# Optimization experiments

Hardware: AMD Instinct MI355X
Metric: run time of the kernel (lower is better)

## Reference

```python
import jax, jax.numpy as jnp
import numpy as np

B, S, D = 4, 2048, 1024
H = 16
DH = D // H  # head dim for qk and v

def setup_inputs() -> dict:
    key = jax.random.key(0)
    ks = jax.random.split(key, 5)
    x_q = jax.random.normal(ks[0], (B, S, D), dtype=jnp.float32)
    # weights stored as [d_in, d_out] (equivalent to torch Linear weight.T)
    scale = 1.0 / np.sqrt(D)
    Wq = jax.random.normal(ks[1], (D, D), dtype=jnp.float32) * scale
    Wk = jax.random.normal(ks[2], (D, D), dtype=jnp.float32) * scale
    Wv = jax.random.normal(ks[3], (D, D), dtype=jnp.float32) * scale
    Wo = jax.random.normal(ks[4], (D, D), dtype=jnp.float32) * scale
    return {"x_q": x_q, "Wq": Wq, "Wk": Wk, "Wv": Wv, "Wo": Wo}

def reference(x_q, Wq, Wk, Wv, Wo):
    b, sq, _ = x_q.shape
    sk = sq  # self-attention: x_k = x_v = x_q
    # projections -> [b, h, s, dh]
    q = (x_q @ Wq).reshape(b, sq, H, DH).transpose(0, 2, 1, 3)
    k = (x_q @ Wk).reshape(b, sk, H, DH).transpose(0, 2, 1, 3)
    v = (x_q @ Wv).reshape(b, sk, H, DH).transpose(0, 2, 1, 3)
    # scores [b, h, sq, sk]
    scores = jnp.einsum('bhqd,bhkd->bhqk', q, k)
    # causal mask: triu(ones(sq, sk), diagonal=1 + sk - sq)
    i = jnp.arange(sq)[:, None]
    j = jnp.arange(sk)[None, :]
    mask = (j - i) >= (1 + sk - sq)
    scores = jnp.where(mask, -jnp.inf, scores)
    attn = jax.nn.softmax(scores / jnp.sqrt(jnp.float32(DH)), axis=-1)
    # dropout p=0.0 -> identity
    ctx = jnp.einsum('bhqk,bhkd->bhqd', attn, v)  # [b,h,sq,dh]
    ctx = ctx.transpose(0, 2, 1, 3).reshape(b, sq, H * DH)
    return ctx @ Wo
```

## Files before the change

kernel.cpp:

```cpp
#include <hip/hip_runtime.h>

#define S_LEN 2048
#define D_MODEL 1024
#define NH 16
#define DHEAD 64
#define BATCH 4

typedef _Float16 half8 __attribute__((ext_vector_type(8)));
typedef __fp16 fp16x2 __attribute__((ext_vector_type(2)));
typedef float floatx4 __attribute__((ext_vector_type(4)));

#define EXP2SCALE 0.1803368801111244f

__device__ __forceinline__ unsigned short f2h(float f) {
    _Float16 h = (_Float16)f;
    return __builtin_bit_cast(unsigned short, h);
}

__device__ __forceinline__ float fexp2(float x) {
    float r;
    asm("v_exp_f32 %0, %1" : "=v"(r) : "v"(x));
    return r;
}
__device__ __forceinline__ float frcp(float x) {
    float r;
    asm("v_rcp_f32 %0, %1" : "=v"(r) : "v"(x));
    return r;
}

__device__ __forceinline__ unsigned int pk2(float a, float b) {
    fp16x2 p = __builtin_amdgcn_cvt_pkrtz(a, b);
    return __builtin_bit_cast(unsigned int, p);
}

__device__ __forceinline__ void gload_lds16(const unsigned short* g, unsigned short* l) {
    __builtin_amdgcn_global_load_lds(
        (const __attribute__((address_space(1))) void*)g,
        (__attribute__((address_space(3))) void*)l,
        16, 0, 0);
}

__global__ __launch_bounds__(256) void convert_f2h_kernel(const float* __restrict__ in,
                                                          unsigned short* __restrict__ out,
                                                          int n4) {
    int i = blockIdx.x * 256 + threadIdx.x;
    if (i < n4) {
        float4 v = ((const float4*)in)[i];
        ushort4 o;
        o.x = f2h(v.x); o.y = f2h(v.y); o.z = f2h(v.z); o.w = f2h(v.w);
        ((ushort4*)out)[i] = o;
    }
}

__global__ __launch_bounds__(256) void transpose_w_kernel(const float* __restrict__ W0,
                                                          const float* __restrict__ W1,
                                                          const float* __restrict__ W2,
                                                          const float* __restrict__ W3,
                                                          unsigned short* __restrict__ T0,
                                                          unsigned short* __restrict__ T1,
                                                          unsigned short* __restrict__ T2,
                                                          unsigned short* __restrict__ T3) {
    const float* W = blockIdx.z == 0 ? W0 : blockIdx.z == 1 ? W1 : blockIdx.z == 2 ? W2 : W3;
    unsigned short* Wt = blockIdx.z == 0 ? T0 : blockIdx.z == 1 ? T1 : blockIdx.z == 2 ? T2 : T3;
    __shared__ float tile[32][33];
    int x = threadIdx.x;
    int y = threadIdx.y;
    int k0 = blockIdx.y * 32;
    int n0 = blockIdx.x * 32;
    for (int i = 0; i < 4; i++)
        tile[y + 8 * i][x] = W[(size_t)(k0 + y + 8 * i) * D_MODEL + n0 + x];
    __syncthreads();
    for (int i = 0; i < 4; i++)
        Wt[(size_t)(n0 + y + 8 * i) * D_MODEL + k0 + x] = f2h(tile[x][y + 8 * i]);
}

template<int MODE>
__device__ __forceinline__ void gemm_body(const unsigned short* __restrict__ A,
                                          const unsigned short* __restrict__ Bt,
                                          void* __restrict__ Cout,
                                          int N, int K,
                                          int bx, int by,
                                          unsigned short* smem, float osc) {
    const int tid  = threadIdx.x;
    const int wave = tid >> 6;
    const int lane = tid & 63;
    const int quad = lane >> 4;
    const int l16  = lane & 15;
    const int wm = (wave >> 1) * 64;
    const int wn = (wave & 1) * 64;
    const int tm = by * 128;
    const int tn = bx * 128;

    const int r0 = tid >> 3;
    const int g0 = (tid & 7) ^ (r0 & 7);
    const unsigned short* pA = A  + (size_t)(tm + r0) * K + g0 * 8;
    const unsigned short* pB = Bt + (size_t)(tn + r0) * K + g0 * 8;
    const int wofs = wave * 512;

    const int sK0 = (((0 << 2) | quad) ^ (l16 & 7)) << 3;
    const int sK1 = (((1 << 2) | quad) ^ (l16 & 7)) << 3;
    const int arow = wm + l16;
    const int brow = wn + l16;

    floatx4 acc[4][4] = {};
    half8 af[2][2], bf[4][2];

    {
        unsigned short* Ab = smem;
        unsigned short* Bb = smem + 8192;
        gload_lds16(pB,         Bb +        wofs);
        gload_lds16(pB + 65536, Bb + 4096 + wofs);
        gload_lds16(pB + 32768, Bb + 2048 + wofs);
        gload_lds16(pB + 98304, Bb + 6144 + wofs);
        gload_lds16(pA,         Ab +        wofs);
        gload_lds16(pA + 65536, Ab + 4096 + wofs);
        gload_lds16(pA + 32768, Ab + 2048 + wofs);
        gload_lds16(pA + 98304, Ab + 6144 + wofs);
        pA += 64; pB += 64;
    }

    for (int t = 0; t < 16; t++) {
        const unsigned short* Ab = smem + (t & 1) * 16384;
        const unsigned short* Bb = Ab + 8192;
        unsigned short* An = smem + ((t & 1) ^ 1) * 16384;
        unsigned short* Bn = An + 8192;
        const bool pf = (t < 15);

        if (pf) {
            gload_lds16(pB,         Bn +        wofs);
            gload_lds16(pB + 65536, Bn + 4096 + wofs);
            asm volatile("s_waitcnt vmcnt(4)" ::: "memory");
        } else {
            asm volatile("s_waitcnt vmcnt(2)" ::: "memory");
        }
        __builtin_amdgcn_s_barrier();
#pragma unroll
        for (int m2 = 0; m2 < 2; m2++) {
            int ro = (arow + m2 * 16) * 64;
            af[m2][0] = *(const half8*)(Ab + ro + sK0);
            af[m2][1] = *(const half8*)(Ab + ro + sK1);
        }
#pragma unroll
        for (int ni = 0; ni < 2; ni++) {
            int ro = (brow + ni * 16) * 64;
            bf[ni][0] = *(const half8*)(Bb + ro + sK0);
            bf[ni][1] = *(const half8*)(Bb + ro + sK1);
        }
        __builtin_amdgcn_s_setprio(1);
#pragma unroll
        for (int m2 = 0; m2 < 2; m2++)
#pragma unroll
            for (int ni = 0; ni < 2; ni++) {
                acc[m2][ni] = __builtin_amdgcn_mfma_f32_16x16x32_f16(af[m2][0], bf[ni][0], acc[m2][ni], 0, 0, 0);
                acc[m2][ni] = __builtin_amdgcn_mfma_f32_16x16x32_f16(af[m2][1], bf[ni][1], acc[m2][ni], 0, 0, 0);
            }
        __builtin_amdgcn_s_setprio(0);

        if (pf) {
            gload_lds16(pB + 32768, Bn + 2048 + wofs);
            gload_lds16(pB + 98304, Bn + 6144 + wofs);
        }
#pragma unroll
        for (int ni = 2; ni < 4; ni++) {
            int ro = (brow + ni * 16) * 64;
            bf[ni][0] = *(const half8*)(Bb + ro + sK0);
            bf[ni][1] = *(const half8*)(Bb + ro + sK1);
        }
        __builtin_amdgcn_s_setprio(1);
#pragma unroll
        for (int m2 = 0; m2 < 2; m2++)
#pragma unroll
            for (int ni = 2; ni < 4; ni++) {
                acc[m2][ni] = __builtin_amdgcn_mfma_f32_16x16x32_f16(af[m2][0], bf[ni][0], acc[m2][ni], 0, 0, 0);
                acc[m2][ni] = __builtin_amdgcn_mfma_f32_16x16x32_f16(af[m2][1], bf[ni][1], acc[m2][ni], 0, 0, 0);
            }
        __builtin_amdgcn_s_setprio(0);

        if (pf) {
            gload_lds16(pA,         An +        wofs);
            gload_lds16(pA + 65536, An + 4096 + wofs);
            asm volatile("s_waitcnt vmcnt(6)" ::: "memory");
        } else {
            asm volatile("s_waitcnt vmcnt(0)" ::: "memory");
        }
        __builtin_amdgcn_s_barrier();
#pragma unroll
        for (int m2 = 0; m2 < 2; m2++) {
            int ro = (arow + (2 + m2) * 16) * 64;
            af[m2][0] = *(const half8*)(Ab + ro + sK0);
            af[m2][1] = *(const half8*)(Ab + ro + sK1);
        }
        __builtin_amdgcn_s_setprio(1);
#pragma unroll
        for (int m2 = 0; m2 < 2; m2++)
#pragma unroll
            for (int ni = 2; ni < 4; ni++) {
                acc[2 + m2][ni] = __builtin_amdgcn_mfma_f32_16x16x32_f16(af[m2][0], bf[ni][0], acc[2 + m2][ni], 0, 0, 0);
                acc[2 + m2][ni] = __builtin_amdgcn_mfma_f32_16x16x32_f16(af[m2][1], bf[ni][1], acc[2 + m2][ni], 0, 0, 0);
            }
        __builtin_amdgcn_s_setprio(0);

        if (pf) {
            gload_lds16(pA + 32768, An + 2048 + wofs);
            gload_lds16(pA + 98304, An + 6144 + wofs);
            pA += 64; pB += 64;
        }
        __builtin_amdgcn_s_setprio(1);
#pragma unroll
        for (int m2 = 0; m2 < 2; m2++)
#pragma unroll
            for (int ni = 0; ni < 2; ni++) {
                acc[2 + m2][ni] = __builtin_amdgcn_mfma_f32_16x16x32_f16(af[m2][0], bf[ni][0], acc[2 + m2][ni], 0, 0, 0);
                acc[2 + m2][ni] = __builtin_amdgcn_mfma_f32_16x16x32_f16(af[m2][1], bf[ni][1], acc[2 + m2][ni], 0, 0, 0);
            }
        __builtin_amdgcn_s_setprio(0);
    }

    if (MODE == 2) {
#pragma unroll
        for (int mi = 0; mi < 4; mi++)
#pragma unroll
            for (int ni = 0; ni < 4; ni++)
#pragma unroll
                for (int r = 0; r < 4; r++) {
                    int row = tm + wm + mi * 16 + quad * 4 + r;
                    int col = tn + wn + ni * 16 + l16;
                    ((float*)Cout)[(size_t)row * N + col] = acc[mi][ni][r];
                }
        return;
    }

    __syncthreads();
    if (MODE == 0) {
#pragma unroll
        for (int mi = 0; mi < 4; mi++)
#pragma unroll
            for (int ni = 0; ni < 4; ni++) {
                int col = wn + ni * 16 + l16;
                int cc  = col >> 4;
                int cil = col & 15;
#pragma unroll
                for (int r = 0; r < 4; r++) {
                    int row = wm + mi * 16 + quad * 4 + r;
                    smem[row * 128 + ((cc ^ ((row >> 2) & 7)) << 4) + cil] = f2h(acc[mi][ni][r] * osc);
                }
            }
        __syncthreads();
        unsigned short* O = (unsigned short*)Cout;
#pragma unroll
        for (int j = 0; j < 8; j++) {
            int vid = tid + j * 256;
            int row = vid >> 4, vv = vid & 15;
            int cc = vv >> 1, hf = vv & 1;
            uint4 v = *(const uint4*)(&smem[row * 128 + ((cc ^ ((row >> 2) & 7)) << 4) + hf * 8]);
            int grow = tm + row;
            int b = grow >> 11, s = grow & 2047;
            int n = tn + vv * 8;
            int h = n >> 6, dh = n & 63;
            *(uint4*)(O + (((size_t)(b * NH + h) * S_LEN + s) * DHEAD + dh)) = v;
        }
    } else {
#pragma unroll
        for (int mi = 0; mi < 4; mi++)
#pragma unroll
            for (int ni = 0; ni < 4; ni++) {
                int col = wn + ni * 16 + l16;
                int sw  = (col >> 2) & 7;
#pragma unroll
                for (int r = 0; r < 4; r++) {
                    int row = wm + mi * 16 + quad * 4 + r;
                    smem[col * 128 + (((row >> 4) ^ sw) << 4) + (row & 15)] = f2h(acc[mi][ni][r]);
                }
            }
        __syncthreads();
        unsigned short* O = (unsigned short*)Cout;
        int b = tm >> 11;
        int sbase = tm & 2047;
#pragma unroll
        for (int j = 0; j < 8; j++) {
            int vid = tid + j * 256;
            int colr = vid >> 4, vv = vid & 15;
            int rc = vv >> 1, hf = vv & 1;
            uint4 v = *(const uint4*)(&smem[colr * 128 + ((rc ^ ((colr >> 2) & 7)) << 4) + hf * 8]);
            int n = tn + colr;
            int h = n >> 6, dh = n & 63;
            *(uint4*)(O + (((size_t)(b * NH + h) * DHEAD + dh) * S_LEN + sbase + vv * 8)) = v;
        }
    }
}

__device__ __forceinline__ void xcd_swz_512(int& bx, int& by) {
    int lin = bx + (by << 3);
    int nl = (lin & 7) * 64 + (lin >> 3);
    bx = nl & 7;
    by = nl >> 3;
}

__global__ __launch_bounds__(256, 2) void qkv_gemm_kernel(const unsigned short* __restrict__ A,
                                                          const unsigned short* __restrict__ Wq,
                                                          const unsigned short* __restrict__ Wk,
                                                          const unsigned short* __restrict__ Wv,
                                                          unsigned short* __restrict__ Qo,
                                                          unsigned short* __restrict__ Ko,
                                                          unsigned short* __restrict__ Vo) {
    __shared__ unsigned short smem[32768];
    int bx = blockIdx.x, by = blockIdx.y;
    xcd_swz_512(bx, by);
    const int z = blockIdx.z;
    if (z == 2)
        gemm_body<1>(A, Wv, Vo, D_MODEL, D_MODEL, bx, by, smem, 1.f);
    else
        gemm_body<0>(A, z == 0 ? Wq : Wk, z == 0 ? Qo : Ko,
                     D_MODEL, D_MODEL, bx, by, smem, z == 0 ? EXP2SCALE : 1.f);
}

__global__ __launch_bounds__(256, 2) void out_gemm_kernel(const unsigned short* __restrict__ A,
                                                          const unsigned short* __restrict__ Bt,
                                                          float* __restrict__ C) {
    __shared__ unsigned short smem[32768];
    int bx = blockIdx.x, by = blockIdx.y;
    xcd_swz_512(bx, by);
    gemm_body<2>(A, Bt, C, D_MODEL, D_MODEL, bx, by, smem, 1.f);
}

__global__ __launch_bounds__(512, 4) void attn_kernel(const unsigned short* __restrict__ Q,
                                                      const unsigned short* __restrict__ K,
                                                      const unsigned short* __restrict__ Vt,
                                                      unsigned short* __restrict__ ctx) {
    __shared__ unsigned short smem[34816];
    unsigned short* Ps = smem + 16384;
    const int tid  = threadIdx.x;
    const int wave = tid >> 6;
    const int wg   = wave >> 2;
    const int wv   = wave & 3;
    const int lane = tid & 63;
    const int quad = lane >> 4;
    const int l16  = lane & 15;
    int lin = blockIdx.x + (blockIdx.y << 3) + (blockIdx.z << 7);
    int nl  = (lin & 7) * 64 + (lin >> 3);
    const int bx = nl & 7;
    const int h  = (nl >> 3) & 15;
    const int b  = nl >> 7;
    const size_t head = (size_t)(b * NH + h) * (S_LEN * DHEAD);

    const int ta = bx, tb = 15 - bx;
    const int tw = wg ? tb : ta;
    const int rounds = 2 * tb + 2;
    const int dk  = 2 * tw + (wv >> 1);
    const int qg0 = tw * 128 + wv * 32 + l16;

    half8 qf[2][2];
#pragma unroll
    for (int s = 0; s < 2; s++)
#pragma unroll
        for (int ks = 0; ks < 2; ks++)
            qf[s][ks] = *(const half8*)(Q + head + (size_t)(qg0 + s * 16) * DHEAD + ks * 32 + quad * 8);

    const int r0 = tid >> 3;
    const int g0 = (tid & 7) ^ (r0 & 7);
    const unsigned short* pK = K  + head + (size_t)r0 * DHEAD + g0 * 8;
    const unsigned short* pV = Vt + head + (size_t)r0 * S_LEN + g0 * 8;
    const int sdst = wave * 512;

    const int akb0 = l16 * 64 + ((quad    ) ^ (l16 & 7)) * 8;
    const int akb1 = l16 * 64 + ((4 | quad) ^ (l16 & 7)) * 8;
    const int psr  = wave * 2304 + l16 * 72;

    floatx4 acc0[4] = {}, acc1[4] = {};
    float l0 = 0.f, l1 = 0.f;

    gload_lds16(pK, smem + sdst);
    gload_lds16(pV, smem + 8192 + sdst);
    pK += 64 * DHEAD; pV += 64;

    for (int c = 0; c < rounds; c++) {
        __syncthreads();
        const int cur = c & 1;
        if (c + 1 < rounds) {
            gload_lds16(pK, smem + (cur ^ 1) * 4096 + sdst);
            gload_lds16(pV, smem + 8192 + (cur ^ 1) * 4096 + sdst);
            pK += 64 * DHEAD; pV += 64;
        }
        if (c > dk) continue;

        const unsigned short* Ksb = smem + cur * 4096;
        const unsigned short* Vsb = smem + 8192 + cur * 4096;

        floatx4 sc0[4] = {}, sc1[4] = {};
#pragma unroll
        for (int ks = 0; ks < 2; ks++) {
            const int ab = ks ? akb1 : akb0;
#pragma unroll
            for (int mk = 0; mk < 4; mk++) {
                half8 ak = *(const half8*)(&Ksb[mk * 1024 + ab]);
                sc0[mk] = __builtin_amdgcn_mfma_f32_16x16x32_f16(ak, qf[0][ks], sc0[mk], 0, 0, 0);
                sc1[mk] = __builtin_amdgcn_mfma_f32_16x16x32_f16(ak, qf[1][ks], sc1[mk], 0, 0, 0);
            }
        }

        const bool diag = (c == dk);

#define SOFTMAX_SET(sc, l_s, qg, setofs)                                          \
        {                                                                         \
            if (diag) {                                                           \
                int rel = (qg) - c * 64 - quad * 4;                               \
                _Pragma("unroll")                                                 \
                for (int mk = 0; mk < 4; mk++)                                    \
                    _Pragma("unroll")                                             \
                    for (int r = 0; r < 4; r++)                                   \
                        if (mk * 16 + r > rel) sc[mk][r] = -3.0e38f;              \
            }                                                                     \
            float rs = 0.f;                                                       \
            _Pragma("unroll")                                                     \
            for (int mk = 0; mk < 4; mk++)                                        \
                _Pragma("unroll")                                                 \
                for (int r = 0; r < 4; r++) {                                     \
                    float e = fexp2(sc[mk][r]);                                   \
                    sc[mk][r] = e;                                                \
                    rs += e;                                                      \
                }                                                                 \
            rs += __shfl_xor(rs, 16, 64);                                         \
            rs += __shfl_xor(rs, 32, 64);                                         \
            l_s += rs;                                                            \
            _Pragma("unroll")                                                     \
            for (int mk = 0; mk < 4; mk++) {                                      \
                uint2 u;                                                          \
                u.x = pk2(sc[mk][0], sc[mk][1]);                                  \
                u.y = pk2(sc[mk][2], sc[mk][3]);                                  \
                *(uint2*)(&Ps[psr + (setofs) + mk * 16 + quad * 4]) = u;          \
            }                                                                     \
        }

        SOFTMAX_SET(sc0, l0, qg0,      0)
        SOFTMAX_SET(sc1, l1, qg0 + 16, 1152)
#undef SOFTMAX_SET

#pragma unroll
        for (int ks = 0; ks < 2; ks++) {
            const int ab = ks ? akb1 : akb0;
            half8 bp0 = *(const half8*)(&Ps[psr        + ks * 32 + quad * 8]);
            half8 bp1 = *(const half8*)(&Ps[psr + 1152 + ks * 32 + quad * 8]);
#pragma unroll
            for (int db = 0; db < 4; db++) {
                half8 av = *(const half8*)(&Vsb[db * 1024 + ab]);
                acc0[db] = __builtin_amdgcn_mfma_f32_16x16x32_f16(av, bp0, acc0[db], 0, 0, 0);
                acc1[db] = __builtin_amdgcn_mfma_f32_16x16x32_f16(av, bp1, acc1[db], 0, 0, 0);
            }
        }
    }

    __syncthreads();
#pragma unroll
    for (int s = 0; s < 2; s++) {
        float inv = frcp(s ? l1 : l0);
        int qrow = wg * 128 + wv * 32 + s * 16 + l16;
        floatx4* ac = s ? acc1 : acc0;
#pragma unroll
        for (int db = 0; db < 4; db++) {
            uint2 u;
            u.x = pk2(ac[db][0] * inv, ac[db][1] * inv);
            u.y = pk2(ac[db][2] * inv, ac[db][3] * inv);
            int chunk = db * 2 + (quad >> 1);
            int sw = chunk ^ (qrow & 7);
            *(uint2*)(&smem[qrow * 64 + sw * 8 + (quad & 1) * 4]) = u;
        }
    }
    __syncthreads();
#pragma unroll
    for (int j = 0; j < 4; j++) {
        int vid = j * 512 + tid;
        int ql = vid >> 3, slot = vid & 7;
        uint4 v = *(const uint4*)(&smem[ql * 64 + slot * 8]);
        int dhc = slot ^ (ql & 7);
        int q = (ql < 128 ? ta * 128 : tb * 128 - 128) + ql;
        *(uint4*)(ctx + ((size_t)b * S_LEN + q) * D_MODEL + h * DHEAD + dhc * 8) = v;
    }
}

extern "C" void kernel_launch(void* const* d_in, const int* in_sizes, int n_in,
                              void* d_out, int out_size, void* d_ws, size_t ws_size,
                              hipStream_t stream) {
    const float* x  = (const float*)d_in[0];
    const float* Wq = (const float*)d_in[1];
    const float* Wk = (const float*)d_in[2];
    const float* Wv = (const float*)d_in[3];
    const float* Wo = (const float*)d_in[4];

    char* ws = (char*)d_ws;
    unsigned short* Xh   = (unsigned short*)(ws + 0);
    unsigned short* Wqt  = (unsigned short*)(ws + 16777216);
    unsigned short* Wkt  = (unsigned short*)(ws + 18874368);
    unsigned short* Wvt  = (unsigned short*)(ws + 20971520);
    unsigned short* Wot  = (unsigned short*)(ws + 23068672);
    unsigned short* Qh   = (unsigned short*)(ws + 25165824);
    unsigned short* Kh   = (unsigned short*)(ws + 41943040);
    unsigned short* Vth  = (unsigned short*)(ws + 58720256);
    unsigned short* ctxh = (unsigned short*)(ws + 75497472);

    const int M = BATCH * S_LEN;

    convert_f2h_kernel<<<(M * D_MODEL / 4 + 255) / 256, 256, 0, stream>>>(x, Xh, M * D_MODEL / 4);
    transpose_w_kernel<<<dim3(32, 32, 4), dim3(32, 8), 0, stream>>>(Wq, Wk, Wv, Wo, Wqt, Wkt, Wvt, Wot);

    qkv_gemm_kernel<<<dim3(8, 64, 3), 256, 0, stream>>>(Xh, Wqt, Wkt, Wvt, Qh, Kh, Vth);

    attn_kernel<<<dim3(8, NH, BATCH), 512, 0, stream>>>(Qh, Kh, Vth, ctxh);

    out_gemm_kernel<<<dim3(8, 64), 256, 0, stream>>>(ctxh, Wot, (float*)d_out);
}
```

Measured before the change: 226.7 us.

## Split final diagonal-band key tiles between work groups to balance causal load

Once wave-group 0 finishes its shorter causal tile range, it reloads Q for group 1's query rows and takes half the key columns (and the matching half of the PV reduction) for the remaining rounds. Group 1 processes the other half. The partial accumulators and row sums are merged through shared memory at the end. The aim is to cut idle time for group 0 in the tail rounds, which group 1 otherwise runs alone. The cost is extra registers for the second accumulator set, extra branching, and an added shared-memory merge with a barrier.

```diff
diff --git a/kernel.cpp b/kernel.cpp
--- a/kernel.cpp
+++ b/kernel.cpp
@@ -346,8 +346,11 @@
     const int ta = bx, tb = 15 - bx;
     const int tw = wg ? tb : ta;
     const int rounds = 2 * tb + 2;
-    const int dk  = 2 * tw + (wv >> 1);
+    const int dkA = 2 * ta + (wv >> 1);
+    const int dkB = 2 * tb + (wv >> 1);
+    const int dkOwn = wg ? dkB : dkA;
     const int qg0 = tw * 128 + wv * 32 + l16;
+    const int qgB = tb * 128 + wv * 32 + l16;
 
     half8 qf[2][2];
 #pragma unroll
@@ -367,7 +370,8 @@
     const int psr  = wave * 2304 + l16 * 72;
 
     floatx4 acc0[4] = {}, acc1[4] = {};
-    float l0 = 0.f, l1 = 0.f;
+    floatx4 accH0[4] = {}, accH1[4] = {};
+    float l0 = 0.f, l1 = 0.f, lH0 = 0.f, lH1 = 0.f;
 
     gload_lds16(pK, smem + sdst);
     gload_lds16(pV, smem + 8192 + sdst);
@@ -381,75 +385,173 @@
             gload_lds16(pV, smem + 8192 + (cur ^ 1) * 4096 + sdst);
             pK += 64 * DHEAD; pV += 64;
         }
-        if (c > dk) continue;
 
         const unsigned short* Ksb = smem + cur * 4096;
         const unsigned short* Vsb = smem + 8192 + cur * 4096;
 
-        floatx4 sc0[4] = {}, sc1[4] = {};
-#pragma unroll
-        for (int ks = 0; ks < 2; ks++) {
-            const int ab = ks ? akb1 : akb0;
-#pragma unroll
-            for (int mk = 0; mk < 4; mk++) {
-                half8 ak = *(const half8*)(&Ksb[mk * 1024 + ab]);
-                sc0[mk] = __builtin_amdgcn_mfma_f32_16x16x32_f16(ak, qf[0][ks], sc0[mk], 0, 0, 0);
-                sc1[mk] = __builtin_amdgcn_mfma_f32_16x16x32_f16(ak, qf[1][ks], sc1[mk], 0, 0, 0);
-            }
-        }
-
-        const bool diag = (c == dk);
+        if (wg == 0 && c == dkA + 1) {
+#pragma unroll
+            for (int s = 0; s < 2; s++)
+#pragma unroll
+                for (int ks = 0; ks < 2; ks++)
+                    qf[s][ks] = *(const half8*)(Q + head + (size_t)(qgB + s * 16) * DHEAD + ks * 32 + quad * 8);
+        }
+
+        if (c <= dkA) {
+            floatx4 sc0[4] = {}, sc1[4] = {};
+#pragma unroll
+            for (int ks = 0; ks < 2; ks++) {
+                const int ab = ks ? akb1 : akb0;
+#pragma unroll
+                for (int mk = 0; mk < 4; mk++) {
+                    half8 ak = *(const half8*)(&Ksb[mk * 1024 + ab]);
+                    sc0[mk] = __builtin_amdgcn_mfma_f32_16x16x32_f16(ak, qf[0][ks], sc0[mk], 0, 0, 0);
+                    sc1[mk] = __builtin_amdgcn_mfma_f32_16x16x32_f16(ak, qf[1][ks], sc1[mk], 0, 0, 0);
+                }
+            }
+            const bool diag = (c == dkOwn);
 
 #define SOFTMAX_SET(sc, l_s, qg, setofs)                                          \
-        {                                                                         \
-            if (diag) {                                                           \
-                int rel = (qg) - c * 64 - quad * 4;                               \
+            {                                                                     \
+                if (diag) {                                                       \
+                    int rel = (qg) - c * 64 - quad * 4;                           \
+                    _Pragma("unroll")                                             \
+                    for (int mk = 0; mk < 4; mk++)                                \
+                        _Pragma("unroll")                                         \
+                        for (int r = 0; r < 4; r++)                               \
+                            if (mk * 16 + r > rel) sc[mk][r] = -3.0e38f;          \
+                }                                                                 \
+                float rs = 0.f;                                                   \
                 _Pragma("unroll")                                                 \
                 for (int mk = 0; mk < 4; mk++)                                    \
                     _Pragma("unroll")                                             \
-                    for (int r = 0; r < 4; r++)                                   \
-                        if (mk * 16 + r > rel) sc[mk][r] = -3.0e38f;              \
-            }                                                                     \
-            float rs = 0.f;                                                       \
-            _Pragma("unroll")                                                     \
-            for (int mk = 0; mk < 4; mk++)                                        \
+                    for (int r = 0; r < 4; r++) {                                 \
+                        float e = fexp2(sc[mk][r]);                               \
+                        sc[mk][r] = e;                                            \
+                        rs += e;                                                  \
+                    }                                                             \
+                rs += __shfl_xor(rs, 16, 64);                                     \
+                rs += __shfl_xor(rs, 32, 64);                                     \
+                l_s += rs;                                                        \
                 _Pragma("unroll")                                                 \
-                for (int r = 0; r < 4; r++) {                                     \
-                    float e = fexp2(sc[mk][r]);                                   \
-                    sc[mk][r] = e;                                                \
-                    rs += e;                                                      \
+                for (int mk = 0; mk < 4; mk++) {                                  \
+                    uint2 u;                                                      \
+                    u.x = pk2(sc[mk][0], sc[mk][1]);                              \
+                    u.y = pk2(sc[mk][2], sc[mk][3]);                              \
+                    *(uint2*)(&Ps[psr + (setofs) + mk * 16 + quad * 4]) = u;      \
                 }                                                                 \
-            rs += __shfl_xor(rs, 16, 64);                                         \
-            rs += __shfl_xor(rs, 32, 64);                                         \
-            l_s += rs;                                                            \
-            _Pragma("unroll")                                                     \
-            for (int mk = 0; mk < 4; mk++) {                                      \
-                uint2 u;                                                          \
-                u.x = pk2(sc[mk][0], sc[mk][1]);                                  \
-                u.y = pk2(sc[mk][2], sc[mk][3]);                                  \
-                *(uint2*)(&Ps[psr + (setofs) + mk * 16 + quad * 4]) = u;          \
-            }                                                                     \
-        }
-
-        SOFTMAX_SET(sc0, l0, qg0,      0)
-        SOFTMAX_SET(sc1, l1, qg0 + 16, 1152)
+            }
+
+            SOFTMAX_SET(sc0, l0, qg0,      0)
+            SOFTMAX_SET(sc1, l1, qg0 + 16, 1152)
 #undef SOFTMAX_SET
 
 #pragma unroll
-        for (int ks = 0; ks < 2; ks++) {
-            const int ab = ks ? akb1 : akb0;
-            half8 bp0 = *(const half8*)(&Ps[psr        + ks * 32 + quad * 8]);
-            half8 bp1 = *(const half8*)(&Ps[psr + 1152 + ks * 32 + quad * 8]);
-#pragma unroll
-            for (int db = 0; db < 4; db++) {
-                half8 av = *(const half8*)(&Vsb[db * 1024 + ab]);
-                acc0[db] = __builtin_amdgcn_mfma_f32_16x16x32_f16(av, bp0, acc0[db], 0, 0, 0);
-                acc1[db] = __builtin_amdgcn_mfma_f32_16x16x32_f16(av, bp1, acc1[db], 0, 0, 0);
+            for (int ks = 0; ks < 2; ks++) {
+                const int ab = ks ? akb1 : akb0;
+                half8 bp0 = *(const half8*)(&Ps[psr        + ks * 32 + quad * 8]);
+                half8 bp1 = *(const half8*)(&Ps[psr + 1152 + ks * 32 + quad * 8]);
+#pragma unroll
+                for (int db = 0; db < 4; db++) {
+                    half8 av = *(const half8*)(&Vsb[db * 1024 + ab]);
+                    acc0[db] = __builtin_amdgcn_mfma_f32_16x16x32_f16(av, bp0, acc0[db], 0, 0, 0);
+                    acc1[db] = __builtin_amdgcn_mfma_f32_16x16x32_f16(av, bp1, acc1[db], 0, 0, 0);
+                }
+            }
+        } else if (c <= dkB) {
+            const int MKB = wg ? 0 : 2;
+            const int KS  = wg ? 0 : 2;
+            const int qgH = wg ? qg0 : qgB;
+            floatx4 s0[2] = {}, s1[2] = {};
+#pragma unroll
+            for (int ks = 0; ks < 2; ks++) {
+                const int ab = ks ? akb1 : akb0;
+#pragma unroll
+                for (int j = 0; j < 2; j++) {
+                    half8 ak = *(const half8*)(&Ksb[(MKB + j) * 1024 + ab]);
+                    s0[j] = __builtin_amdgcn_mfma_f32_16x16x32_f16(ak, qf[0][ks], s0[j], 0, 0, 0);
+                    s1[j] = __builtin_amdgcn_mfma_f32_16x16x32_f16(ak, qf[1][ks], s1[j], 0, 0, 0);
+                }
+            }
+            if (c == dkB) {
+                int rel = qgH - c * 64 - quad * 4;
+#pragma unroll
+                for (int j = 0; j < 2; j++)
+#pragma unroll
+                    for (int r = 0; r < 4; r++) {
+                        if ((MKB + j) * 16 + r > rel)      s0[j][r] = -3.0e38f;
+                        if ((MKB + j) * 16 + r > rel + 16) s1[j][r] = -3.0e38f;
+                    }
+            }
+            float rs0 = 0.f, rs1 = 0.f;
+#pragma unroll
+            for (int j = 0; j < 2; j++)
+#pragma unroll
+                for (int r = 0; r < 4; r++) {
+                    float e0 = fexp2(s0[j][r]); s0[j][r] = e0; rs0 += e0;
+                    float e1 = fexp2(s1[j][r]); s1[j][r] = e1; rs1 += e1;
+                }
+            rs0 += __shfl_xor(rs0, 16, 64); rs0 += __shfl_xor(rs0, 32, 64);
+            rs1 += __shfl_xor(rs1, 16, 64); rs1 += __shfl_xor(rs1, 32, 64);
+            if (wg) { l0 += rs0; l1 += rs1; } else { lH0 += rs0; lH1 += rs1; }
+#pragma unroll
+            for (int j = 0; j < 2; j++) {
+                uint2 u0, u1;
+                u0.x = pk2(s0[j][0], s0[j][1]); u0.y = pk2(s0[j][2], s0[j][3]);
+                u1.x = pk2(s1[j][0], s1[j][1]); u1.y = pk2(s1[j][2], s1[j][3]);
+                *(uint2*)(&Ps[psr        + (MKB + j) * 16 + quad * 4]) = u0;
+                *(uint2*)(&Ps[psr + 1152 + (MKB + j) * 16 + quad * 4]) = u1;
+            }
+            {
+                const int ab = wg ? akb0 : akb1;
+                half8 bp0 = *(const half8*)(&Ps[psr        + KS * 16 + quad * 8]);
+                half8 bp1 = *(const half8*)(&Ps[psr + 1152 + KS * 16 + quad * 8]);
+#pragma unroll
+                for (int db = 0; db < 4; db++) {
+                    half8 av = *(const half8*)(&Vsb[db * 1024 + ab]);
+                    if (wg) {
+                        acc0[db] = __builtin_amdgcn_mfma_f32_16x16x32_f16(av, bp0, acc0[db], 0, 0, 0);
+                        acc1[db] = __builtin_amdgcn_mfma_f32_16x16x32_f16(av, bp1, acc1[db], 0, 0, 0);
+                    } else {
+                        accH0[db] = __builtin_amdgcn_mfma_f32_16x16x32_f16(av, bp0, accH0[db], 0, 0, 0);
+                        accH1[db] = __builtin_amdgcn_mfma_f32_16x16x32_f16(av, bp1, accH1[db], 0, 0, 0);
+                    }
+                }
             }
         }
     }
 
     __syncthreads();
+    float* mrg = (float*)(smem + 16384);
+    float* lm  = mrg + 8192;
+    if (wg == 0) {
+        int base = wave * 2048 + lane * 16;
+#pragma unroll
+        for (int db = 0; db < 4; db++)
+#pragma unroll
+            for (int r = 0; r < 4; r++) {
+                mrg[base + db * 4 + r]        = accH0[db][r];
+                mrg[base + 1024 + db * 4 + r] = accH1[db][r];
+            }
+        if (quad == 0) {
+            lm[wave * 32 + l16]      = lH0;
+            lm[wave * 32 + 16 + l16] = lH1;
+        }
+    }
+    __syncthreads();
+    if (wg == 1) {
+        int base = (wave - 4) * 2048 + lane * 16;
+#pragma unroll
+        for (int db = 0; db < 4; db++)
+#pragma unroll
+            for (int r = 0; r < 4; r++) {
+                acc0[db][r] += mrg[base + db * 4 + r];
+                acc1[db][r] += mrg[base + 1024 + db * 4 + r];
+            }
+        l0 += lm[(wave - 4) * 32 + l16];
+        l1 += lm[(wave - 4) * 32 + 16 + l16];
+    }
+
 #pragma unroll
     for (int s = 0; s < 2; s++) {
         float inv = frcp(s ? l1 : l0);
```

Result: slower. 300.5 us (+32.5%).

## Enlarge GEMM block tile to 256x128 with 512 threads sharing B tile

Applied to the files above, without the earlier changes.

The QKV and output GEMMs now use 256x128 block tiles computed by 8 waves (512 threads) instead of 128x128 tiles with 4 waves, halving the grid along M. Each loaded B tile is reused by twice as many rows, which cuts global and L2 traffic per FLOP. The LDS buffers, prefetch schedule, waitcnt values, epilogue swizzles and XCD block remapping are rewritten to match. The cost is more LDS per block (96 KB), fewer blocks in the grid, and possible occupancy and tail-wave effects.

```diff
diff --git a/kernel.cpp b/kernel.cpp
--- a/kernel.cpp
+++ b/kernel.cpp
@@ -86,9 +86,9 @@
     const int lane = tid & 63;
     const int quad = lane >> 4;
     const int l16  = lane & 15;
-    const int wm = (wave >> 1) * 64;
-    const int wn = (wave & 1) * 64;
-    const int tm = by * 128;
+    const int wr = wave >> 1;
+    const int wc = wave & 1;
+    const int tm = by * 256;
     const int tn = bx * 128;
 
     const int r0 = tid >> 3;
@@ -97,52 +97,47 @@
     const unsigned short* pB = Bt + (size_t)(tn + r0) * K + g0 * 8;
     const int wofs = wave * 512;
 
-    const int sK0 = (((0 << 2) | quad) ^ (l16 & 7)) << 3;
-    const int sK1 = (((1 << 2) | quad) ^ (l16 & 7)) << 3;
-    const int arow = wm + l16;
-    const int brow = wn + l16;
+    const int sK0 = ((      quad) ^ (l16 & 7)) << 3;
+    const int sK1 = (((4 | quad)) ^ (l16 & 7)) << 3;
 
     floatx4 acc[4][4] = {};
     half8 af[2][2], bf[4][2];
 
     {
-        unsigned short* Ab = smem;
-        unsigned short* Bb = smem + 8192;
-        gload_lds16(pB,         Bb +        wofs);
-        gload_lds16(pB + 65536, Bb + 4096 + wofs);
-        gload_lds16(pB + 32768, Bb + 2048 + wofs);
-        gload_lds16(pB + 98304, Bb + 6144 + wofs);
-        gload_lds16(pA,         Ab +        wofs);
-        gload_lds16(pA + 65536, Ab + 4096 + wofs);
-        gload_lds16(pA + 32768, Ab + 2048 + wofs);
-        gload_lds16(pA + 98304, Ab + 6144 + wofs);
+        unsigned short* Ab0 = smem;
+        unsigned short* Bb0 = smem + 16384;
+        gload_lds16(pB,          Bb0 +        wofs);
+        gload_lds16(pB + 65536,  Bb0 + 4096 + wofs);
+        gload_lds16(pA,          Ab0 +        wofs);
+        gload_lds16(pA + 65536,  Ab0 + 4096 + wofs);
+        gload_lds16(pA + 131072, Ab0 + 8192 + wofs);
+        gload_lds16(pA + 196608, Ab0 + 12288 + wofs);
         pA += 64; pB += 64;
     }
 
     for (int t = 0; t < 16; t++) {
-        const unsigned short* Ab = smem + (t & 1) * 16384;
-        const unsigned short* Bb = Ab + 8192;
-        unsigned short* An = smem + ((t & 1) ^ 1) * 16384;
-        unsigned short* Bn = An + 8192;
+        const unsigned short* Ab = smem + (t & 1) * 24576;
+        const unsigned short* Bb = Ab + 16384;
+        unsigned short* Nb = smem + ((t & 1) ^ 1) * 24576;
         const bool pf = (t < 15);
 
         if (pf) {
-            gload_lds16(pB,         Bn +        wofs);
-            gload_lds16(pB + 65536, Bn + 4096 + wofs);
-            asm volatile("s_waitcnt vmcnt(4)" ::: "memory");
+            gload_lds16(pB,         Nb + 16384 +        wofs);
+            gload_lds16(pB + 65536, Nb + 16384 + 4096 + wofs);
+            asm volatile("s_waitcnt vmcnt(2)" ::: "memory");
         } else {
-            asm volatile("s_waitcnt vmcnt(2)" ::: "memory");
+            asm volatile("s_waitcnt vmcnt(0)" ::: "memory");
         }
         __builtin_amdgcn_s_barrier();
 #pragma unroll
         for (int m2 = 0; m2 < 2; m2++) {
-            int ro = (arow + m2 * 16) * 64;
+            int ro = (wr * 64 + m2 * 16 + l16) * 64;
             af[m2][0] = *(const half8*)(Ab + ro + sK0);
             af[m2][1] = *(const half8*)(Ab + ro + sK1);
         }
 #pragma unroll
         for (int ni = 0; ni < 2; ni++) {
-            int ro = (brow + ni * 16) * 64;
+            int ro = (wc * 64 + ni * 16 + l16) * 64;
             bf[ni][0] = *(const half8*)(Bb + ro + sK0);
             bf[ni][1] = *(const half8*)(Bb + ro + sK1);
         }
@@ -157,12 +152,12 @@
         __builtin_amdgcn_s_setprio(0);
 
         if (pf) {
-            gload_lds16(pB + 32768, Bn + 2048 + wofs);
-            gload_lds16(pB + 98304, Bn + 6144 + wofs);
+            gload_lds16(pA,         Nb +        wofs);
+            gload_lds16(pA + 65536, Nb + 4096 + wofs);
         }
 #pragma unroll
         for (int ni = 2; ni < 4; ni++) {
-            int ro = (brow + ni * 16) * 64;
+            int ro = (wc * 64 + ni * 16 + l16) * 64;
             bf[ni][0] = *(const half8*)(Bb + ro + sK0);
             bf[ni][1] = *(const half8*)(Bb + ro + sK1);
         }
@@ -177,16 +172,13 @@
         __builtin_amdgcn_s_setprio(0);
 
         if (pf) {
-            gload_lds16(pA,         An +        wofs);
-            gload_lds16(pA + 65536, An + 4096 + wofs);
-            asm volatile("s_waitcnt vmcnt(6)" ::: "memory");
-        } else {
-            asm volatile("s_waitcnt vmcnt(0)" ::: "memory");
+            gload_lds16(pA + 131072, Nb + 8192 + wofs);
+            gload_lds16(pA + 196608, Nb + 12288 + wofs);
         }
         __builtin_amdgcn_s_barrier();
 #pragma unroll
         for (int m2 = 0; m2 < 2; m2++) {
-            int ro = (arow + (2 + m2) * 16) * 64;
+            int ro = (wr * 64 + 32 + m2 * 16 + l16) * 64;
             af[m2][0] = *(const half8*)(Ab + ro + sK0);
             af[m2][1] = *(const half8*)(Ab + ro + sK1);
         }
@@ -200,11 +192,7 @@
             }
         __builtin_amdgcn_s_setprio(0);
 
-        if (pf) {
-            gload_lds16(pA + 32768, An + 2048 + wofs);
-            gload_lds16(pA + 98304, An + 6144 + wofs);
-            pA += 64; pB += 64;
-        }
+        if (pf) { pA += 64; pB += 64; }
         __builtin_amdgcn_s_setprio(1);
 #pragma unroll
         for (int m2 = 0; m2 < 2; m2++)
@@ -223,8 +211,8 @@
             for (int ni = 0; ni < 4; ni++)
 #pragma unroll
                 for (int r = 0; r < 4; r++) {
-                    int row = tm + wm + mi * 16 + quad * 4 + r;
-                    int col = tn + wn + ni * 16 + l16;
+                    int row = tm + wr * 64 + mi * 16 + quad * 4 + r;
+                    int col = tn + wc * 64 + ni * 16 + l16;
                     ((float*)Cout)[(size_t)row * N + col] = acc[mi][ni][r];
                 }
         return;
@@ -236,12 +224,12 @@
         for (int mi = 0; mi < 4; mi++)
 #pragma unroll
             for (int ni = 0; ni < 4; ni++) {
-                int col = wn + ni * 16 + l16;
+                int col = wc * 64 + ni * 16 + l16;
                 int cc  = col >> 4;
                 int cil = col & 15;
 #pragma unroll
                 for (int r = 0; r < 4; r++) {
-                    int row = wm + mi * 16 + quad * 4 + r;
+                    int row = wr * 64 + mi * 16 + quad * 4 + r;
                     smem[row * 128 + ((cc ^ ((row >> 2) & 7)) << 4) + cil] = f2h(acc[mi][ni][r] * osc);
                 }
             }
@@ -249,7 +237,7 @@
         unsigned short* O = (unsigned short*)Cout;
 #pragma unroll
         for (int j = 0; j < 8; j++) {
-            int vid = tid + j * 256;
+            int vid = tid + j * 512;
             int row = vid >> 4, vv = vid & 15;
             int cc = vv >> 1, hf = vv & 1;
             uint4 v = *(const uint4*)(&smem[row * 128 + ((cc ^ ((row >> 2) & 7)) << 4) + hf * 8]);
@@ -264,12 +252,12 @@
         for (int mi = 0; mi < 4; mi++)
 #pragma unroll
             for (int ni = 0; ni < 4; ni++) {
-                int col = wn + ni * 16 + l16;
-                int sw  = (col >> 2) & 7;
+                int col = wc * 64 + ni * 16 + l16;
+                int sw  = (col >> 2) & 15;
 #pragma unroll
                 for (int r = 0; r < 4; r++) {
-                    int row = wm + mi * 16 + quad * 4 + r;
-                    smem[col * 128 + (((row >> 4) ^ sw) << 4) + (row & 15)] = f2h(acc[mi][ni][r]);
+                    int row = wr * 64 + mi * 16 + quad * 4 + r;
+                    smem[col * 256 + (((row >> 4) ^ sw) << 4) + (row & 15)] = f2h(acc[mi][ni][r]);
                 }
             }
         __syncthreads();
@@ -278,10 +266,10 @@
         int sbase = tm & 2047;
 #pragma unroll
         for (int j = 0; j < 8; j++) {
-            int vid = tid + j * 256;
-            int colr = vid >> 4, vv = vid & 15;
+            int vid = tid + j * 512;
+            int colr = vid >> 5, vv = vid & 31;
             int rc = vv >> 1, hf = vv & 1;
-            uint4 v = *(const uint4*)(&smem[colr * 128 + ((rc ^ ((colr >> 2) & 7)) << 4) + hf * 8]);
+            uint4 v = *(const uint4*)(&smem[colr * 256 + ((rc ^ ((colr >> 2) & 15)) << 4) + hf * 8]);
             int n = tn + colr;
             int h = n >> 6, dh = n & 63;
             *(uint4*)(O + (((size_t)(b * NH + h) * DHEAD + dh) * S_LEN + sbase + vv * 8)) = v;
@@ -289,23 +277,23 @@
     }
 }
 
-__device__ __forceinline__ void xcd_swz_512(int& bx, int& by) {
-    int lin = bx + (by << 3);
-    int nl = (lin & 7) * 64 + (lin >> 3);
-    bx = nl & 7;
-    by = nl >> 3;
-}
-
-__global__ __launch_bounds__(256, 2) void qkv_gemm_kernel(const unsigned short* __restrict__ A,
+__device__ __forceinline__ void xcd_swz_256(int& bx, int& by) {
+    int d = bx + (by << 3);
+    int c = d & 7, i = d >> 3;
+    by = c * 4 + (i >> 3);
+    bx = i & 7;
+}
+
+__global__ __launch_bounds__(512, 2) void qkv_gemm_kernel(const unsigned short* __restrict__ A,
                                                           const unsigned short* __restrict__ Wq,
                                                           const unsigned short* __restrict__ Wk,
                                                           const unsigned short* __restrict__ Wv,
                                                           unsigned short* __restrict__ Qo,
                                                           unsigned short* __restrict__ Ko,
                                                           unsigned short* __restrict__ Vo) {
-    __shared__ unsigned short smem[32768];
+    __shared__ unsigned short smem[49152];
     int bx = blockIdx.x, by = blockIdx.y;
-    xcd_swz_512(bx, by);
+    xcd_swz_256(bx, by);
     const int z = blockIdx.z;
     if (z == 2)
         gemm_body<1>(A, Wv, Vo, D_MODEL, D_MODEL, bx, by, smem, 1.f);
@@ -314,12 +302,12 @@
                      D_MODEL, D_MODEL, bx, by, smem, z == 0 ? EXP2SCALE : 1.f);
 }
 
-__global__ __launch_bounds__(256, 2) void out_gemm_kernel(const unsigned short* __restrict__ A,
+__global__ __launch_bounds__(512, 2) void out_gemm_kernel(const unsigned short* __restrict__ A,
                                                           const unsigned short* __restrict__ Bt,
                                                           float* __restrict__ C) {
-    __shared__ unsigned short smem[32768];
+    __shared__ unsigned short smem[49152];
     int bx = blockIdx.x, by = blockIdx.y;
-    xcd_swz_512(bx, by);
+    xcd_swz_256(bx, by);
     gemm_body<2>(A, Bt, C, D_MODEL, D_MODEL, bx, by, smem, 1.f);
 }
 
@@ -502,9 +490,9 @@
     convert_f2h_kernel<<<(M * D_MODEL / 4 + 255) / 256, 256, 0, stream>>>(x, Xh, M * D_MODEL / 4);
     transpose_w_kernel<<<dim3(32, 32, 4), dim3(32, 8), 0, stream>>>(Wq, Wk, Wv, Wo, Wqt, Wkt, Wvt, Wot);
 
-    qkv_gemm_kernel<<<dim3(8, 64, 3), 256, 0, stream>>>(Xh, Wqt, Wkt, Wvt, Qh, Kh, Vth);
+    qkv_gemm_kernel<<<dim3(8, 32, 3), 512, 0, stream>>>(Xh, Wqt, Wkt, Wvt, Qh, Kh, Vth);
 
     attn_kernel<<<dim3(8, NH, BATCH), 512, 0, stream>>>(Qh, Kh, Vth, ctxh);
 
-    out_gemm_kernel<<<dim3(8, 64), 256, 0, stream>>>(ctxh, Wot, (float*)d_out);
-}
+    out_gemm_kernel<<<dim3(8, 32), 512, 0, stream>>>(ctxh, Wot, (float*)d_out);
+}
```

Measured after the change: 230.9 us. About the same (+1.8%).
